# Optimization experiments

Hardware: AMD Instinct MI355X
Metric: run time of the kernel (lower is better)

## Reference

```python
import jax, jax.numpy as jnp
import numpy as np

T, A, C = 32, 64, 3            # steps, image side (A==B), channels
RN, WN = 5, 5                  # read/write glimpse sizes
Z, ENC, DEC = 100, 512, 512    # latent, encoder, decoder sizes
LIN, LH, AL = 300, 128, 512    # lang input, lang hidden, align hidden
BATCH, L = 128, 32             # batch, caption length


def lstm_cell(xt, h, c, Wih, Whh, bih, bhh):
    # torch.nn.LSTMCell gate order: i, f, g, o
    g = xt @ Wih.T + h @ Whh.T + bih + bhh
    i, f, gg, o = jnp.split(g, 4, axis=-1)
    c2 = jax.nn.sigmoid(f) * c + jax.nn.sigmoid(i) * jnp.tanh(gg)
    return jax.nn.sigmoid(o) * jnp.tanh(c2), c2


def bi_lstm(y, Wf, Uf, bf1, bf2, Wb, Ub, bb1, bb2):
    Bsz, H = y.shape[0], Uf.shape[1]
    xs = jnp.swapaxes(y, 0, 1)  # [L,B,LIN]
    z = jnp.zeros((Bsz, H), y.dtype)
    def mk(Wih, Whh, bih, bhh):
        def step(carry, xt):
            h, c = carry
            h2, c2 = lstm_cell(xt, h, c, Wih, Whh, bih, bhh)
            return (h2, c2), h2
        return step
    _, hf = jax.lax.scan(mk(Wf, Uf, bf1, bf2), (z, z), xs)
    _, hb = jax.lax.scan(mk(Wb, Ub, bb1, bb2), (z, z), xs, reverse=True)
    return jnp.concatenate([jnp.swapaxes(hf, 0, 1), jnp.swapaxes(hb, 0, 1)], axis=-1)


def filterbank(gx, gy, sigma2, delta, N):
    grid = jnp.arange(N, dtype=jnp.float32)[None]          # [1,N]
    mu_x = gx + (grid - N / 2 - 0.5) * delta               # [b,N]
    mu_y = gy + (grid - N / 2 - 0.5) * delta
    a = jnp.arange(A, dtype=jnp.float32)                   # [A] (A==B)
    s2 = sigma2[:, :, None]                                # [b,1,1]
    Fx = jnp.exp(-(a[None, None, :] - mu_x[:, :, None]) ** 2 / (2 * s2))
    Fy = jnp.exp(-(a[None, None, :] - mu_y[:, :, None]) ** 2 / (2 * s2))
    Fx = Fx / (Fx.sum(2, keepdims=True) + 1e-8)
    Fy = Fy / (Fy.sum(2, keepdims=True) + 1e-8)
    return Fx, Fy                                          # [b,N,A]


def attn_window(h, W, b, N):
    p = h @ W.T + b                                        # [b,5]
    gx_, gy_, ls2, ld, lg = [p[:, i:i + 1] for i in range(5)]
    gx = (A + 1) / 2 * (gx_ + 1)
    gy = (A + 1) / 2 * (gy_ + 1)
    delta = (A - 1) / (N - 1) * jnp.exp(ld)
    Fx, Fy = filterbank(gx, gy, jnp.exp(ls2), delta, N)
    return Fx, Fy, jnp.exp(lg)


def setup_inputs() -> dict:
    key = jax.random.key(0)
    ki = iter(jax.random.split(key, 64))
    def p(shape, s=0.05):
        return s * jax.random.normal(next(ki), shape, dtype=jnp.float32)
    z = lambda *s: jnp.zeros(s, jnp.float32)
    inp = {}
    inp['x'] = jax.random.uniform(next(ki), (BATCH, C * A * A), dtype=jnp.float32)
    inp['y'] = p((BATCH, L, LIN), 1.0)
    inp['eps_q'] = p((T, BATCH, Z), 1.0)
    inp['enc_Wih'] = p((4 * ENC, 2 * RN * RN * C + DEC)); inp['enc_Whh'] = p((4 * ENC, ENC))
    inp['enc_bih'] = z(4 * ENC); inp['enc_bhh'] = z(4 * ENC)
    inp['dec_Wih'] = p((4 * DEC, Z + 2 * LH)); inp['dec_Whh'] = p((4 * DEC, DEC))
    inp['dec_bih'] = z(4 * DEC); inp['dec_bhh'] = z(4 * DEC)
    inp['mu_W'] = p((Z, ENC)); inp['mu_b'] = z(Z)
    inp['sig_W'] = p((Z, ENC)); inp['sig_b'] = z(Z)
    inp['write_W'] = p((WN * WN * C, DEC)); inp['write_b'] = z(WN * WN * C)
    inp['align_W1'] = p((AL, 2 * LH + DEC)); inp['align_b1'] = z(AL)
    inp['align_w2'] = p((1, AL))
    inp['attn_W'] = p((5, DEC)); inp['attn_b'] = z(5)
    inp['lf_Wih'] = p((4 * LH, LIN)); inp['lf_Whh'] = p((4 * LH, LH))
    inp['lf_bih'] = z(4 * LH); inp['lf_bhh'] = z(4 * LH)
    inp['lb_Wih'] = p((4 * LH, LIN)); inp['lb_Whh'] = p((4 * LH, LH))
    inp['lb_bih'] = z(4 * LH); inp['lb_bhh'] = z(4 * LH)
    return inp


def reference(x, y, eps_q, enc_Wih, enc_Whh, enc_bih, enc_bhh, dec_Wih, dec_Whh,
              dec_bih, dec_bhh, mu_W, mu_b, sig_W, sig_b, write_W, write_b,
              align_W1, align_b1, align_w2, attn_W, attn_b,
              lf_Wih, lf_Whh, lf_bih, lf_bhh, lb_Wih, lb_Whh, lb_bih, lb_bhh):
    Bsz = x.shape[0]
    h_lang = bi_lstm(y, lf_Wih, lf_Whh, lf_bih, lf_bhh, lb_Wih, lb_Whh, lb_bih, lb_bhh)  # [b,L,2LH]
    x_img = x.reshape(Bsz, C, A, A)
    # original code never updates c_prev for t>0 (no-op line), so c_prev == 0 always
    xhat_img = x_img - 0.5  # x - sigmoid(0)

    def step(carry, eps):
        h_enc, c_enc, h_dec, c_dec = carry
        # read glimpse with Gaussian filterbank from previous decoder state
        Fx, Fy, gamma = attn_window(h_dec, attn_W, attn_b, RN)
        def glimpse(img):
            g = jnp.einsum('biy,bcyx,bjx->bcij', Fy, img, Fx)  # [b,C,RN,RN]
            return g.reshape(Bsz, RN * RN * C) * gamma
        r = jnp.concatenate([glimpse(x_img), glimpse(xhat_img)], axis=1)
        h_enc2, c_enc2 = lstm_cell(jnp.concatenate([r, h_dec], 1), h_enc, c_enc,
                                   enc_Wih, enc_Whh, enc_bih, enc_bhh)
        mu = h_enc2 @ mu_W.T + mu_b
        q = mu + eps * jnp.exp(h_enc2 @ sig_W.T + sig_b)
        # alignment attention over language states (exp/normalize == softmax)
        ain = jnp.concatenate([jnp.broadcast_to(h_dec[:, None, :], (Bsz, h_lang.shape[1], DEC)), h_lang], -1)
        logits = jnp.tanh(ain @ align_W1.T + align_b1) @ align_w2.T  # [b,L,1]
        sent = jnp.sum(h_lang * jax.nn.softmax(logits, axis=1), axis=1)
        h_dec2, c_dec2 = lstm_cell(jnp.concatenate([q, sent], 1), h_dec, c_dec,
                                   dec_Wih, dec_Whh, dec_bih, dec_bhh)
        # write glimpse
        w = (h_dec2 @ write_W.T + write_b).reshape(Bsz, C, WN, WN)
        Fxw, Fyw, gw = attn_window(h_dec2, attn_W, attn_b, WN)
        wr = jnp.einsum('biy,bcij,bjx->bcyx', Fyw, w, Fxw).reshape(Bsz, C * A * A) / gw
        return (h_enc2, c_enc2, h_dec2, c_dec2), wr  # cs[t] = 0 + write

    ze = jnp.zeros((Bsz, ENC), x.dtype)
    zd = jnp.zeros((Bsz, DEC), x.dtype)
    _, cs = jax.lax.scan(step, (ze, ze, zd, zd), eps_q)
    return cs  # [T, b, C*A*A]
```

## Files before the change

kernel.cpp:

```cpp
#include <hip/hip_runtime.h>
#include <hip/hip_bf16.h>
#include <math.h>

typedef __attribute__((ext_vector_type(8))) short short8;
typedef __attribute__((ext_vector_type(4))) float floatx4;

__device__ __forceinline__ float sigmoidf_(float v){ return 1.f/(1.f+expf(-v)); }

__device__ __forceinline__ floatx4 mfma16(short8 a, short8 b, floatx4 c) {
    return __builtin_amdgcn_mfma_f32_16x16x32_bf16(a, b, c, 0, 0, 0);
}

__device__ __forceinline__ void store3(__hip_bfloat16* p, long row, int kp, int col, float v){
    __hip_bfloat16 hi = __float2bfloat16(v);
    float lo = v - __bfloat162float(hi);
    p[row + col]        = hi;
    p[row + kp + col]   = __float2bfloat16(lo);
    p[row + 2*kp + col] = hi;
}

#define MFMA_TILE_BODY \
    { const short8* A8 = (const short8*)sA; \
      const short8* B8 = (const short8*)sB; \
      short8 a0 = A8[l], a1 = A8[64+l]; \
      short8 b0 = B8[(w*2)*64 + l], b1 = B8[(w*2+1)*64 + l]; \
      acc[0][0] = mfma16(a0,b0,acc[0][0]); \
      acc[0][1] = mfma16(a0,b1,acc[0][1]); \
      acc[1][0] = mfma16(a1,b0,acc[1][0]); \
      acc[1][1] = mfma16(a1,b1,acc[1][1]); }

#define MFMA_TILE_BODY2 \
    { const short8* A8 = (const short8*)sA; \
      const short8* B8 = (const short8*)sB; \
      short8 a0 = A8[l], a1 = A8[64+l]; \
      short8 b0 = B8[(w*2)*64 + l], b1 = B8[(w*2+1)*64 + l]; \
      acc[0][0] = mfma16(a0,b0,acc[0][0]); \
      acc[0][1] = mfma16(a0,b1,acc[0][1]); \
      acc[1][0] = mfma16(a1,b0,acc[1][0]); \
      acc[1][1] = mfma16(a1,b1,acc[1][1]); \
      short8 c0 = A8[128+l], c1 = A8[192+l]; \
      short8 d0 = B8[512+(w*2)*64 + l], d1 = B8[512+(w*2+1)*64 + l]; \
      acc[0][0] = mfma16(c0,d0,acc[0][0]); \
      acc[0][1] = mfma16(c0,d1,acc[0][1]); \
      acc[1][0] = mfma16(c1,d0,acc[1][0]); \
      acc[1][1] = mfma16(c1,d1,acc[1][1]); }

__device__ void mfma_loop_32x128(const __hip_bfloat16* Apk, long lda, int m0,
                                 const __hip_bfloat16* Wrows, long ldb,
                                 int KS, char* sA, char* sB, floatx4 acc[2][2])
{
    const int tid = threadIdx.x, l = tid & 63, w = tid >> 6;
    const char* Ab = (const char*)(Apk + (long)(m0 + (tid>>6)*16 + (tid&15))*lda
                                   + (long)(((tid&63)>>4)*8));
    int r0 = tid >> 2, qd = tid & 3;
    const char* Bb0 = (const char*)(Wrows + (long)r0*ldb + qd*8);
    const char* Bb1 = (const char*)(Wrows + (long)(r0+64)*ldb + qd*8);
    int4* sAv = (int4*)sA;
    int4* sBv = (int4*)sB;
    int bs0 = (r0>>4)*64 + (r0&15) + (qd<<4);
    int bs1 = bs0 + 256;
    const int NIT = KS >> 1, tail = KS & 1;
    int4 aE0,aE1,b0E0,b0E1,b1E0,b1E1;
    int4 aO0,aO1,b0O0,b0O1,b1O0,b1O1;
    if (NIT > 0) {
        if (tid < 128) { aE0 = *(const int4*)Ab; aE1 = *(const int4*)(Ab+64); }
        b0E0 = *(const int4*)Bb0; b0E1 = *(const int4*)(Bb0+64);
        b1E0 = *(const int4*)Bb1; b1E1 = *(const int4*)(Bb1+64);
    }
    if (NIT > 1) {
        if (tid < 128) { aO0 = *(const int4*)(Ab+128); aO1 = *(const int4*)(Ab+192); }
        b0O0 = *(const int4*)(Bb0+128); b0O1 = *(const int4*)(Bb0+192);
        b1O0 = *(const int4*)(Bb1+128); b1O1 = *(const int4*)(Bb1+192);
    }
    int it = 0;
    for (; it + 1 < NIT; it += 2) {
        __syncthreads();
        if (tid < 128) { sAv[tid] = aE0; sAv[128+tid] = aE1; }
        sBv[bs0] = b0E0; sBv[bs1] = b1E0; sBv[512+bs0] = b0E1; sBv[512+bs1] = b1E1;
        __syncthreads();
        if (it + 2 < NIT) {
            long off = (long)(it+2)*128;
            if (tid < 128) { aE0 = *(const int4*)(Ab+off); aE1 = *(const int4*)(Ab+off+64); }
            b0E0 = *(const int4*)(Bb0+off); b0E1 = *(const int4*)(Bb0+off+64);
            b1E0 = *(const int4*)(Bb1+off); b1E1 = *(const int4*)(Bb1+off+64);
        }
        MFMA_TILE_BODY2
        __syncthreads();
        if (tid < 128) { sAv[tid] = aO0; sAv[128+tid] = aO1; }
        sBv[bs0] = b0O0; sBv[bs1] = b1O0; sBv[512+bs0] = b0O1; sBv[512+bs1] = b1O1;
        __syncthreads();
        if (it + 3 < NIT) {
            long off = (long)(it+3)*128;
            if (tid < 128) { aO0 = *(const int4*)(Ab+off); aO1 = *(const int4*)(Ab+off+64); }
            b0O0 = *(const int4*)(Bb0+off); b0O1 = *(const int4*)(Bb0+off+64);
            b1O0 = *(const int4*)(Bb1+off); b1O1 = *(const int4*)(Bb1+off+64);
        }
        MFMA_TILE_BODY2
    }
    if (it < NIT) {
        __syncthreads();
        if (tid < 128) { sAv[tid] = aE0; sAv[128+tid] = aE1; }
        sBv[bs0] = b0E0; sBv[bs1] = b1E0; sBv[512+bs0] = b0E1; sBv[512+bs1] = b1E1;
        __syncthreads();
        MFMA_TILE_BODY2
    }
    if (tail) {
        long off = (long)NIT*128;
        int4 aT, bT0, bT1;
        if (tid < 128) aT = *(const int4*)(Ab+off);
        bT0 = *(const int4*)(Bb0+off); bT1 = *(const int4*)(Bb1+off);
        __syncthreads();
        if (tid < 128) sAv[tid] = aT;
        sBv[bs0] = bT0; sBv[bs1] = bT1;
        __syncthreads();
        MFMA_TILE_BODY
    }
}

__device__ void gemm_tile(const __hip_bfloat16* Apk, long lda, int m0,
                          const __hip_bfloat16* Wpk, long ldb, int n0,
                          const float* b1, const float* b2,
                          void* Cout, long ldc, int KS, int out_bf16, char* smem)
{
    char* sA = smem; char* sB = smem + 4096;
    floatx4 z4 = {0.f,0.f,0.f,0.f};
    floatx4 acc[2][2] = {{z4,z4},{z4,z4}};
    mfma_loop_32x128(Apk, lda, m0, Wpk + (long)n0*ldb, ldb, KS, sA, sB, acc);
    const int tid = threadIdx.x, l = tid&63, w = tid>>6;
    for (int i = 0; i < 2; ++i)
      for (int jn = 0; jn < 2; ++jn) {
        int n = n0 + (w*2+jn)*16 + (l&15);
        float bb = (b1? b1[n]:0.f) + (b2? b2[n]:0.f);
        for (int r = 0; r < 4; ++r) {
            int m = m0 + i*16 + ((l>>4)<<2) + r;
            float v = acc[i][jn][r] + bb;
            if (out_bf16) ((__hip_bfloat16*)Cout)[(long)m*ldc + n] = __float2bfloat16(v);
            else          ((float*)Cout)[(long)m*ldc + n] = v;
        }
      }
}

__global__ __launch_bounds__(256)
void gemm_mfma_k(const __hip_bfloat16* Apk, long lda,
                 const __hip_bfloat16* Bpk, long ldb,
                 const float* b1, const float* b2,
                 void* Cout, long ldc, int KS, int out_bf16)
{
    __shared__ __align__(16) char smem[20480];
    gemm_tile(Apk, lda, blockIdx.x*32, Bpk, ldb, blockIdx.y*128, b1, b2,
              Cout, ldc, KS, out_bf16, smem);
}

__device__ void gates_cell_tile(const __hip_bfloat16* Apk, long lda,
                                const __hip_bfloat16* Wpk, long ldw,
                                const float* bpk, float* c_state, float* h_f32,
                                __hip_bfloat16* d1, int d1ld, int d1kp, int d1off,
                                __hip_bfloat16* d2, int d2ld, int d2kp, int d2off,
                                __hip_bfloat16* d3, int d3ld, int d3kp, int d3off,
                                int KS, int m0, int jb, char* smem)
{
    char* sA = smem; char* sB = smem + 4096;
    floatx4 z4 = {0.f,0.f,0.f,0.f};
    floatx4 acc[2][2] = {{z4,z4},{z4,z4}};
    mfma_loop_32x128(Apk, lda, m0, Wpk + (long)jb*128*ldw, ldw, KS, sA, sB, acc);
    __syncthreads();
    float (*gl)[36] = (float(*)[36])smem;
    const int tid = threadIdx.x, l = tid&63, w = tid>>6;
    for (int i = 0; i < 2; ++i)
      for (int jn = 0; jn < 2; ++jn) {
        int nl = (w*2+jn)*16 + (l&15);
        int mb = i*16 + ((l>>4)<<2);
        *(floatx4*)&gl[nl][mb] = acc[i][jn];
      }
    __syncthreads();
    for (int idx = tid; idx < 1024; idx += 256) {
        int u = idx >> 5, m = idx & 31;
        float g0 = gl[u   ][m] + bpk[jb*128 + u];
        float g1 = gl[32+u][m] + bpk[jb*128 + 32 + u];
        float g2 = gl[64+u][m] + bpk[jb*128 + 64 + u];
        float g3 = gl[96+u][m] + bpk[jb*128 + 96 + u];
        int bg = m0 + m, un = jb*32 + u;
        long ci = (long)bg*512 + un;
        float c2 = sigmoidf_(g1)*c_state[ci] + sigmoidf_(g0)*tanhf(g2);
        float h2 = sigmoidf_(g3)*tanhf(c2);
        c_state[ci] = c2;
        if (h_f32) h_f32[ci] = h2;
        store3(d1, (long)bg*d1ld, d1kp, d1off + un, h2);
        if (d2) store3(d2, (long)bg*d2ld, d2kp, d2off + un, h2);
        if (d3) store3(d3, (long)bg*d3ld, d3kp, d3off + un, h2);
    }
}

__device__ void align_fn(int b, const float* dp, const float* langpre,
                         const float* hlang, const float* w2,
                         __hip_bfloat16* Ad_p, char* smem)
{
    float* dps    = (float*)smem;
    float* red    = dps + 512;
    float* logits = red + 256;
    float* smv    = logits + 32;
    float* ssum   = smv + 32;
    const int tid = threadIdx.x;
    for (int k = tid; k < 512; k += 256) dps[k] = dp[(long)b*512 + k];
    __syncthreads();
    {
        int ll = tid >> 3, part = tid & 7;
        const float* lp = langpre + ((long)b*32 + ll)*512 + part*64;
        const float* dpp = dps + part*64;
        const float* w2p = w2 + part*64;
        float acc = 0.f;
        for (int a = 0; a < 64; ++a)
            acc += tanhf(dpp[a] + lp[a]) * w2p[a];
        red[tid] = acc;
    }
    __syncthreads();
    if ((tid & 7) == 0) {
        float s = 0.f;
        for (int p2 = 0; p2 < 8; ++p2) s += red[tid + p2];
        logits[tid >> 3] = s;
    }
    __syncthreads();
    if (tid == 0) {
        float mx = logits[0];
        for (int i = 1; i < 32; ++i) mx = fmaxf(mx, logits[i]);
        float s = 0.f;
        for (int i = 0; i < 32; ++i) { float e = expf(logits[i]-mx); smv[i]=e; s+=e; }
        ssum[0] = s;
    }
    __syncthreads();
    {
        float acc = 0.f;
        const float* hl = hlang + (long)b*32*256 + tid;
        for (int i = 0; i < 32; ++i) acc += smv[i]*hl[(long)i*256];
        store3(Ad_p, (long)b*2688, 896, 104 + tid, acc/ssum[0]);
    }
}

__global__ __launch_bounds__(256)
void enc_align_k(const __hip_bfloat16* Ae_p, const __hip_bfloat16* Wenc,
                 const float* benc, float* c_enc,
                 __hip_bfloat16* Ae_q, __hip_bfloat16* Ahe3,
                 const float* dp, const float* langpre, const float* hlang,
                 const float* w2, __hip_bfloat16* Ad_p)
{
    __shared__ __align__(16) char smem[20480];
    int bid = blockIdx.x;
    if (bid < 64) {
        int m0 = ((bid>>4)&3)*32, jb = bid & 15;
        gates_cell_tile(Ae_p, 3552, Wenc, 3552, benc, c_enc, nullptr,
                        Ae_q, 3552, 1184, 664,  Ahe3, 1536, 512, 0,
                        nullptr, 0, 0, 0,  111, m0, jb, smem);
    } else {
        align_fn(bid-64, dp, langpre, hlang, w2, Ad_p, smem);
    }
}

__global__ __launch_bounds__(256)
void dec_k(const __hip_bfloat16* Ad_p, const __hip_bfloat16* Wdec, const float* bdec,
           float* c_dec, float* h_dec,
           __hip_bfloat16* Ae_q, __hip_bfloat16* Ad_q, __hip_bfloat16* Ahd3)
{
    __shared__ __align__(16) char smem[20480];
    int m0 = ((blockIdx.x>>4)&3)*32, jb = blockIdx.x & 15;
    gates_cell_tile(Ad_p, 2688, Wdec, 2688, bdec, c_dec, h_dec,
                    Ae_q, 3552, 1184, 152,  Ad_q, 2688, 896, 360,
                    Ahd3, 1536, 512, 0,  84, m0, jb, smem);
}

__global__ __launch_bounds__(256)
void musig_k(const __hip_bfloat16* Ahe3, const __hip_bfloat16* Wms3,
             const float* mu_b, const float* sig_b,
             const float* eps, __hip_bfloat16* Ad_p)
{
    __shared__ __align__(16) char smem[20480];
    char* sA = smem; char* sB = smem + 4096;
    floatx4 z4 = {0.f,0.f,0.f,0.f};
    floatx4 acc[2][2] = {{z4,z4},{z4,z4}};
    int m0 = blockIdx.x*32, n0 = blockIdx.y*128, base = blockIdx.y*64;
    mfma_loop_32x128(Ahe3, 1536, m0, Wms3 + (long)n0*1536, 1536, 48, sA, sB, acc);
    __syncthreads();
    float (*gl)[36] = (float(*)[36])smem;
    const int tid = threadIdx.x, l = tid&63, w = tid>>6;
    for (int i = 0; i < 2; ++i)
      for (int jn = 0; jn < 2; ++jn) {
        int nl = (w*2+jn)*16 + (l&15);
        int mb = i*16 + ((l>>4)<<2);
        *(floatx4*)&gl[nl][mb] = acc[i][jn];
      }
    __syncthreads();
    for (int idx = tid; idx < 2048; idx += 256) {
        int u = idx >> 5, m = idx & 31;
        int o = base + u;
        if (o >= 100) continue;
        int bg = m0 + m;
        float mu = gl[u][m] + mu_b[o];
        float sg = expf(gl[64+u][m] + sig_b[o]);
        float q = mu + eps[(long)bg*100 + o]*sg;
        store3(Ad_p, (long)bg*2688, 896, o, q);
    }
}

__device__ void attn_params5(const float* hd, const float* attn_W, const float* attn_b,
                             float* sP, float* scratch)
{
    const int tid = threadIdx.x;
    float p0=0.f,p1=0.f,p2=0.f,p3=0.f,p4=0.f;
    for (int k = tid; k < 512; k += 256) {
        float v = hd[k];
        p0 += v*attn_W[k];      p1 += v*attn_W[512+k];  p2 += v*attn_W[1024+k];
        p3 += v*attn_W[1536+k]; p4 += v*attn_W[2048+k];
    }
    for (int off = 32; off; off >>= 1) {
        p0 += __shfl_down(p0, off); p1 += __shfl_down(p1, off);
        p2 += __shfl_down(p2, off); p3 += __shfl_down(p3, off);
        p4 += __shfl_down(p4, off);
    }
    if ((tid & 63) == 0) {
        int wv = tid >> 6;
        scratch[wv*5+0]=p0; scratch[wv*5+1]=p1; scratch[wv*5+2]=p2;
        scratch[wv*5+3]=p3; scratch[wv*5+4]=p4;
    }
    __syncthreads();
    if (tid < 5) sP[tid] = scratch[tid]+scratch[5+tid]+scratch[10+tid]+scratch[15+tid]+attn_b[tid];
    __syncthreads();
}

__device__ void glimpse_fn(int b, const float* x, const float* h_dec,
                           const float* attn_W, const float* attn_b,
                           __hip_bfloat16* Ae_q, char* smem)
{
    float* red = (float*)smem;
    float* sP  = red + 256;
    float* Fx  = sP + 8;
    float* Fy  = Fx + 320;
    float* denx= Fy + 320;
    float* deny= denx + 8;
    float* SFx = deny + 8;
    float* SFy = SFx + 8;
    float* tmp1= SFy + 8;
    const int tid = threadIdx.x;
    attn_params5(h_dec + (long)b*512, attn_W, attn_b, sP, red);
    float gx    = 32.5f*(sP[0]+1.f);
    float gy    = 32.5f*(sP[1]+1.f);
    float s2    = expf(sP[2]);
    float delta = 15.75f*expf(sP[3]);
    for (int p = tid; p < 320; p += 256) {
        int i = p >> 6, a = p & 63;
        float mux = gx + ((float)i - 3.0f)*delta;
        float muy = gy + ((float)i - 3.0f)*delta;
        float dx = (float)a - mux, dy = (float)a - muy;
        Fx[i*64+a] = expf(-dx*dx/(2.f*s2));
        Fy[i*64+a] = expf(-dy*dy/(2.f*s2));
    }
    __syncthreads();
    if (tid < 10) {
        int i = tid % 5;
        const float* F = (tid < 5) ? (Fx + i*64) : (Fy + i*64);
        float s = 0.f;
        for (int a = 0; a < 64; ++a) s += F[a];
        if (tid < 5) denx[i] = s + 1e-8f; else deny[i] = s + 1e-8f;
    }
    __syncthreads();
    for (int p = tid; p < 320; p += 256) {
        int i = p >> 6, a = p & 63;
        Fx[i*64+a] /= denx[i];
        Fy[i*64+a] /= deny[i];
    }
    __syncthreads();
    if (tid < 10) {
        int i = tid % 5;
        const float* F = (tid < 5) ? (Fx + i*64) : (Fy + i*64);
        float s = 0.f;
        for (int a = 0; a < 64; ++a) s += F[a];
        if (tid < 5) SFx[i] = s; else SFy[i] = s;
    }
    __syncthreads();
    for (int p = tid; p < 192; p += 256) {
        int cc = p / 64, yy = p - cc*64;
        const float* row = x + (long)b*12288 + cc*4096 + yy*64;
        float a0=0,a1=0,a2=0,a3=0,a4=0;
        for (int xx = 0; xx < 64; ++xx) {
            float v = row[xx];
            a0 += v*Fx[0*64+xx]; a1 += v*Fx[1*64+xx]; a2 += v*Fx[2*64+xx];
            a3 += v*Fx[3*64+xx]; a4 += v*Fx[4*64+xx];
        }
        tmp1[(cc*64+yy)*5+0]=a0; tmp1[(cc*64+yy)*5+1]=a1; tmp1[(cc*64+yy)*5+2]=a2;
        tmp1[(cc*64+yy)*5+3]=a3; tmp1[(cc*64+yy)*5+4]=a4;
    }
    __syncthreads();
    if (tid < 75) {
        int cc = tid/25, i = (tid/5)%5, j = tid%5;
        float g = 0.f;
        for (int yy = 0; yy < 64; ++yy) g += Fy[i*64+yy]*tmp1[(cc*64+yy)*5 + j];
        float gamma = expf(sP[4]);
        long ro = (long)b*3552;
        store3(Ae_q, ro, 1184, tid,      gamma*g);
        store3(Ae_q, ro, 1184, 75 + tid, gamma*(g - 0.5f*SFy[i]*SFx[j]));
    }
}

__device__ void write_fn(int b, const float* h_dec,
                         const float* write_W, const float* write_b,
                         const float* attn_W, const float* attn_b,
                         float* outp, char* smem)
{
    float* hs  = (float*)smem;
    float* red = hs + 512;
    float* sP  = red + 256;
    float* w75 = sP + 8;
    float* Fx  = w75 + 80;
    float* Fy  = Fx + 320;
    float* denx= Fy + 320;
    float* deny= denx + 8;
    float* t2  = deny + 8;
    const int tid = threadIdx.x;
    for (int k = tid; k < 512; k += 256) hs[k] = h_dec[(long)b*512 + k];
    __syncthreads();
    attn_params5(hs, attn_W, attn_b, sP, red);
    float gx    = 32.5f*(sP[0]+1.f);
    float gy    = 32.5f*(sP[1]+1.f);
    float s2    = expf(sP[2]);
    float delta = 15.75f*expf(sP[3]);
    float inv_g = 1.f/expf(sP[4]);
    if (tid < 75) {
        const float4* w4 = (const float4*)(write_W + (long)tid*512);
        const float4* h4 = (const float4*)hs;
        float acc = 0.f;
        for (int k = 0; k < 128; ++k) {
            float4 wv = w4[k], hv = h4[k];
            acc += wv.x*hv.x + wv.y*hv.y + wv.z*hv.z + wv.w*hv.w;
        }
        w75[tid] = acc + write_b[tid];
    }
    for (int p = tid; p < 320; p += 256) {
        int i = p >> 6, a = p & 63;
        float mux = gx + ((float)i - 3.0f)*delta;
        float muy = gy + ((float)i - 3.0f)*delta;
        float dx = (float)a - mux, dy = (float)a - muy;
        Fx[i*64+a] = expf(-dx*dx/(2.f*s2));
        Fy[i*64+a] = expf(-dy*dy/(2.f*s2));
    }
    __syncthreads();
    if (tid < 10) {
        int i = tid % 5;
        const float* F = (tid < 5) ? (Fx + i*64) : (Fy + i*64);
        float s = 0.f;
        for (int a = 0; a < 64; ++a) s += F[a];
        if (tid < 5) denx[i] = s + 1e-8f; else deny[i] = s + 1e-8f;
    }
    __syncthreads();
    for (int p = tid; p < 320; p += 256) {
        int i = p >> 6, a = p & 63;
        Fx[i*64+a] /= denx[i];
        Fy[i*64+a] /= deny[i];
    }
    __syncthreads();
    for (int p = tid; p < 960; p += 256) {
        int cc = p / 320, rem = p - cc*320;
        int i = rem / 64, xx = rem - i*64;
        float acc = 0.f;
        for (int j = 0; j < 5; ++j) acc += w75[cc*25 + i*5 + j]*Fx[j*64+xx];
        t2[(cc*5+i)*64+xx] = acc;
    }
    __syncthreads();
    float* ob = outp + (long)b*12288;
    for (int p = tid; p < 12288; p += 256) {
        int cc = p >> 12, yy = (p >> 6) & 63, xx = p & 63;
        float acc = 0.f;
        for (int i = 0; i < 5; ++i) acc += Fy[i*64+yy]*t2[(cc*5+i)*64+xx];
        ob[p] = acc*inv_g;
    }
}

__global__ __launch_bounds__(256)
void wgd_k(const float* x, const float* h_dec,
           const float* attn_W, const float* attn_b,
           const float* write_W, const float* write_b,
           float* outp,
           __hip_bfloat16* Ae_q,
           const __hip_bfloat16* Ahd3, const __hip_bfloat16* W1dec3,
           float* dp)
{
    __shared__ __align__(16) char smem[20480];
    int bid = blockIdx.x;
    if (bid < 128) {
        glimpse_fn(bid, x, h_dec, attn_W, attn_b, Ae_q, smem);
    } else if (bid < 144) {
        int t = bid - 128;
        gemm_tile(Ahd3, 1536, (t&3)*32, W1dec3, 1536, (t>>2)*128,
                  nullptr, nullptr, dp, 512, 48, 0, smem);
    } else {
        if (outp) write_fn(bid-144, h_dec, write_W, write_b, attn_W, attn_b, outp, smem);
    }
}

__global__ __launch_bounds__(512)
void lang_all_k(const float* xpf, const float* xpb,
                const float* Whh_f, const float* Whh_b,
                float* hlang)
{
    const int pr  = blockIdx.x & 63;
    const int dir = blockIdx.x >> 6;
    const int tid = threadIdx.x;
    const int b0  = pr*2;
    const float* Whh = dir ? Whh_b : Whh_f;
    const float* xps = dir ? xpb : xpf;
    __shared__ __align__(16) float hs[2][128];
    __shared__ float gs[2][512];
    float4 wr[32];
    {
        const float4* w4 = (const float4*)(Whh + (long)tid*128);
        #pragma unroll
        for (int k = 0; k < 32; ++k) wr[k] = w4[k];
    }
    if (tid < 256) hs[tid>>7][tid&127] = 0.f;
    float cst = 0.f;
    __syncthreads();
    for (int s = 0; s < 32; ++s) {
        const int l = dir ? (31 - s) : s;
        const float4* h40 = (const float4*)hs[0];
        const float4* h41 = (const float4*)hs[1];
        float a0 = 0.f, a1 = 0.f;
        #pragma unroll
        for (int k = 0; k < 32; ++k) {
            float4 wv = wr[k], h0 = h40[k], h1 = h41[k];
            a0 += wv.x*h0.x + wv.y*h0.y + wv.z*h0.z + wv.w*h0.w;
            a1 += wv.x*h1.x + wv.y*h1.y + wv.z*h1.z + wv.w*h1.w;
        }
        gs[0][tid] = a0 + xps[((long)b0*32 + l)*512 + tid];
        gs[1][tid] = a1 + xps[((long)(b0+1)*32 + l)*512 + tid];
        __syncthreads();
        if (tid < 256) {
            int bb = tid >> 7, u = tid & 127;
            float c2 = sigmoidf_(gs[bb][128+u])*cst + sigmoidf_(gs[bb][u])*tanhf(gs[bb][256+u]);
            float h2 = sigmoidf_(gs[bb][384+u])*tanhf(c2);
            cst = c2;
            hlang[((long)(b0+bb)*32 + l)*256 + dir*128 + u] = h2;
            hs[bb][u] = h2;
        }
        __syncthreads();
    }
}

__global__ void pack_a3_k(__hip_bfloat16* dst, int KP, long N,
                          const float* src, int ld, int K1)
{
    long idx = (long)blockIdx.x*256 + threadIdx.x;
    int K3 = 3*KP;
    long tot = N*K3;
    if (idx >= tot) return;
    long n = idx / K3; int k3 = (int)(idx - n*K3);
    int plane = k3 / KP, k = k3 - plane*KP;
    float v = (k < K1) ? src[n*ld + k] : 0.f;
    __hip_bfloat16 hi = __float2bfloat16(v);
    float lo = v - __bfloat162float(hi);
    dst[idx] = (plane==1) ? __float2bfloat16(lo) : hi;
}

__global__ void pack_w3_k(__hip_bfloat16* dst, int KP, long N,
                          const float* src, int ld, int K1)
{
    long idx = (long)blockIdx.x*256 + threadIdx.x;
    int K3 = 3*KP;
    long tot = N*K3;
    if (idx >= tot) return;
    long n = idx / K3; int k3 = (int)(idx - n*K3);
    int plane = k3 / KP, k = k3 - plane*KP;
    float v = (k < K1) ? src[n*ld + k] : 0.f;
    __hip_bfloat16 hi = __float2bfloat16(v);
    float lo = v - __bfloat162float(hi);
    dst[idx] = (plane==2) ? __float2bfloat16(lo) : hi;
}

__global__ void pack_gates3_k(__hip_bfloat16* dst, int KP,
                              const float* Wih, int ldih, int K1, int off2, int K2, int off3,
                              const float* Whh)
{
    long idx = (long)blockIdx.x*256 + threadIdx.x;
    int K3 = 3*KP;
    long tot = 2048L*K3;
    if (idx >= tot) return;
    long p = idx / K3; int k3 = (int)(idx - p*K3);
    int plane = k3 / KP, k = k3 - plane*KP;
    int j = (int)(p >> 7), g = (int)((p>>5)&3), uu = (int)(p&31);
    int n = g*512 + j*32 + uu;
    float v = 0.f;
    if (k < K1)                          v = Wih[(long)n*ldih + k];
    else if (k >= off2 && k < off2+K2)   v = Wih[(long)n*ldih + K1 + (k-off2)];
    else if (k >= off3 && k < off3+512)  v = Whh[(long)n*512 + (k-off3)];
    __hip_bfloat16 hi = __float2bfloat16(v);
    float lo = v - __bfloat162float(hi);
    dst[idx] = (plane==2) ? __float2bfloat16(lo) : hi;
}

__global__ void pack_gbias_k(float* dst, const float* bih, const float* bhh)
{
    int p = blockIdx.x*256 + threadIdx.x;
    if (p >= 2048) return;
    int j = p >> 7, g = (p>>5)&3, uu = p&31;
    int n = g*512 + j*32 + uu;
    dst[p] = bih[n] + bhh[n];
}

__global__ void pack_musig3_k(__hip_bfloat16* dst, const float* mu_W, const float* sig_W)
{
    long idx = (long)blockIdx.x*256 + threadIdx.x;
    if (idx >= 256L*1536) return;
    int p = (int)(idx / 1536), k3 = (int)(idx - (long)p*1536);
    int plane = k3 >> 9, k = k3 & 511;
    int u = p & 127, base = (p >> 7)*64;
    int z = base + (u & 63);
    const float* W = (u < 64) ? mu_W : sig_W;
    float v = (z < 100) ? W[(long)z*512 + k] : 0.f;
    __hip_bfloat16 hi = __float2bfloat16(v);
    float lo = v - __bfloat162float(hi);
    dst[idx] = (plane==2) ? __float2bfloat16(lo) : hi;
}

extern "C" void kernel_launch(void* const* d_in, const int* in_sizes, int n_in,
                              void* d_out, int out_size, void* d_ws, size_t ws_size,
                              hipStream_t stream)
{
    const float* x        = (const float*)d_in[0];
    const float* y        = (const float*)d_in[1];
    const float* eps_q    = (const float*)d_in[2];
    const float* enc_Wih  = (const float*)d_in[3];
    const float* enc_Whh  = (const float*)d_in[4];
    const float* enc_bih  = (const float*)d_in[5];
    const float* enc_bhh  = (const float*)d_in[6];
    const float* dec_Wih  = (const float*)d_in[7];
    const float* dec_Whh  = (const float*)d_in[8];
    const float* dec_bih  = (const float*)d_in[9];
    const float* dec_bhh  = (const float*)d_in[10];
    const float* mu_W     = (const float*)d_in[11];
    const float* mu_b     = (const float*)d_in[12];
    const float* sig_W    = (const float*)d_in[13];
    const float* sig_b    = (const float*)d_in[14];
    const float* write_W  = (const float*)d_in[15];
    const float* write_b  = (const float*)d_in[16];
    const float* align_W1 = (const float*)d_in[17];
    const float* align_b1 = (const float*)d_in[18];
    const float* align_w2 = (const float*)d_in[19];
    const float* attn_W   = (const float*)d_in[20];
    const float* attn_b   = (const float*)d_in[21];
    const float* lf_Wih   = (const float*)d_in[22];
    const float* lf_Whh   = (const float*)d_in[23];
    const float* lf_bih   = (const float*)d_in[24];
    const float* lf_bhh   = (const float*)d_in[25];
    const float* lb_Wih   = (const float*)d_in[26];
    const float* lb_Whh   = (const float*)d_in[27];
    const float* lb_bih   = (const float*)d_in[28];
    const float* lb_bhh   = (const float*)d_in[29];
    float* out = (float*)d_out;

    float* ws = (float*)d_ws;
    size_t off = 0;
    auto alloc = [&](size_t n){ float* p = ws + off; off += n; return p; };

    float* Aenc0f = alloc(227328);
    float* Aenc1f = alloc(227328);
    float* Adec0f = alloc(172032);
    float* Adec1f = alloc(172032);
    float* Ahd3f  = alloc(98304);
    float* Ahe3f  = alloc(98304);
    float* c_enc  = alloc(65536);
    float* c_dec  = alloc(65536);
    float* h_dec  = alloc(65536);
    size_t zero_floats = off;
    float* dpb      = alloc(65536);
    float* hlangf   = alloc(1048576);
    float* hlang3f  = alloc(1572864);
    float* langpre  = alloc(2097152);
    float* W1lang3f = alloc(196608);
    float* W1dec3f  = alloc(393216);
    float* shared = alloc(6651904);
    float* y3f   = shared;
    float* Wlf3f = shared + 1966080;
    float* Wlb3f = Wlf3f + 245760;
    float* xpf   = Wlb3f + 245760;
    float* xpb   = xpf + 2097152;
    float* Wenc3f = shared;
    float* Wdec3f = Wenc3f + 3637248;
    float* Wms3f  = Wdec3f + 2752512;
    float* benc   = Wms3f + 196608;
    float* bdec   = benc + 2048;

    __hip_bfloat16* Aenc0 = (__hip_bfloat16*)Aenc0f;
    __hip_bfloat16* Aenc1 = (__hip_bfloat16*)Aenc1f;
    __hip_bfloat16* Adec0 = (__hip_bfloat16*)Adec0f;
    __hip_bfloat16* Adec1 = (__hip_bfloat16*)Adec1f;
    __hip_bfloat16* Ahd3  = (__hip_bfloat16*)Ahd3f;
    __hip_bfloat16* Ahe3  = (__hip_bfloat16*)Ahe3f;
    __hip_bfloat16* hlang3= (__hip_bfloat16*)hlang3f;
    __hip_bfloat16* W1lang3=(__hip_bfloat16*)W1lang3f;
    __hip_bfloat16* W1dec3= (__hip_bfloat16*)W1dec3f;
    __hip_bfloat16* y3    = (__hip_bfloat16*)y3f;
    __hip_bfloat16* Wlf3  = (__hip_bfloat16*)Wlf3f;
    __hip_bfloat16* Wlb3  = (__hip_bfloat16*)Wlb3f;
    __hip_bfloat16* Wenc3 = (__hip_bfloat16*)Wenc3f;
    __hip_bfloat16* Wdec3 = (__hip_bfloat16*)Wdec3f;
    __hip_bfloat16* Wms3  = (__hip_bfloat16*)Wms3f;

    hipMemsetAsync(ws, 0, zero_floats*sizeof(float), stream);

    pack_a3_k<<<(4096L*960+255)/256,256,0,stream>>>(y3, 320, 4096, y, 300, 300);
    pack_w3_k<<<(512L*960+255)/256,256,0,stream>>>(Wlf3, 320, 512, lf_Wih, 300, 300);
    pack_w3_k<<<(512L*960+255)/256,256,0,stream>>>(Wlb3, 320, 512, lb_Wih, 300, 300);
    pack_w3_k<<<(512L*768+255)/256,256,0,stream>>>(W1lang3, 256, 512, align_W1+512, 768, 256);
    pack_w3_k<<<(512L*1536+255)/256,256,0,stream>>>(W1dec3, 512, 512, align_W1, 768, 512);
    gemm_mfma_k<<<dim3(128,4),256,0,stream>>>(y3, 960, Wlf3, 960, lf_bih, lf_bhh, xpf, 512, 30, 0);
    gemm_mfma_k<<<dim3(128,4),256,0,stream>>>(y3, 960, Wlb3, 960, lb_bih, lb_bhh, xpb, 512, 30, 0);
    lang_all_k<<<128,512,0,stream>>>(xpf, xpb, lf_Whh, lb_Whh, hlangf);
    pack_a3_k<<<(4096L*768+255)/256,256,0,stream>>>(hlang3, 256, 4096, hlangf, 256, 256);
    gemm_mfma_k<<<dim3(128,4),256,0,stream>>>(hlang3, 768, W1lang3, 768, align_b1, nullptr, langpre, 512, 24, 0);

    pack_gates3_k<<<(2048L*10656+255)/256,256,0,stream>>>(Wenc3, 1184, enc_Wih, 662, 150, 152, 512, 664, enc_Whh);
    pack_gates3_k<<<(2048L*8064+255)/256,256,0,stream>>>(Wdec3, 896, dec_Wih, 356, 100, 104, 256, 360, dec_Whh);
    pack_gbias_k<<<8,256,0,stream>>>(benc, enc_bih, enc_bhh);
    pack_gbias_k<<<8,256,0,stream>>>(bdec, dec_bih, dec_bhh);
    pack_musig3_k<<<(256L*1536+255)/256,256,0,stream>>>(Wms3, mu_W, sig_W);

    wgd_k<<<272,256,0,stream>>>(x, h_dec, attn_W, attn_b, write_W, write_b,
                                nullptr, Aenc0, Ahd3, W1dec3, dpb);

    for (int t = 0; t < 32; ++t) {
        int p = t & 1;
        __hip_bfloat16* Ae_p = p ? Aenc1 : Aenc0;
        __hip_bfloat16* Ae_q = p ? Aenc0 : Aenc1;
        __hip_bfloat16* Ad_p = p ? Adec1 : Adec0;
        __hip_bfloat16* Ad_q = p ? Adec0 : Adec1;
        enc_align_k<<<192,256,0,stream>>>(Ae_p, Wenc3, benc, c_enc, Ae_q, Ahe3,
                                          dpb, langpre, hlangf, align_w2, Ad_p);
        musig_k<<<dim3(4,2),256,0,stream>>>(Ahe3, Wms3, mu_b, sig_b,
                                            eps_q + (long)t*12800, Ad_p);
        dec_k<<<64,256,0,stream>>>(Ad_p, Wdec3, bdec, c_dec, h_dec, Ae_q, Ad_q, Ahd3);
        wgd_k<<<272,256,0,stream>>>(x, h_dec, attn_W, attn_b, write_W, write_b,
                                    out + (long)t*128*12288, Ae_q, Ahd3, W1dec3, dpb);
    }
}
```

Measured before the change: 4.117 ms.

## Split-K the recurrent LSTM gate and mu/sigma GEMMs across two blocks

The encoder, decoder and mu/sigma GEMM tiles now split K across two blocks. Each block writes its partial accumulators to global memory, and an atomic counter picks the last-arriving block to add the other half and run the epilogue. This doubles the number of blocks per step in the latency-bound recurrent loop, at the cost of partial-sum traffic, fences and per-step counter arrays. The glimpse read loop is also vectorized with float4 loads, and the pack kernels use a 2D grid so the per-element 64-bit divisions go away.

```diff
diff --git a/kernel.cpp b/kernel.cpp
--- a/kernel.cpp
+++ b/kernel.cpp
@@ -117,6 +117,30 @@
     }
 }
 
+__device__ int splitk_handoff(floatx4 acc[2][2], float* partial, int* cnt,
+                              int tile, int half)
+{
+    const int tid = threadIdx.x;
+    float* pb = partial + ((long)tile*2 + half)*4096 + tid*16;
+    *(floatx4*)(pb)    = acc[0][0];
+    *(floatx4*)(pb+4)  = acc[0][1];
+    *(floatx4*)(pb+8)  = acc[1][0];
+    *(floatx4*)(pb+12) = acc[1][1];
+    __threadfence();
+    __shared__ int who;
+    __syncthreads();
+    if (tid == 0) who = atomicAdd(&cnt[tile], 1);
+    __syncthreads();
+    if (who == 0) return 0;
+    __threadfence();
+    const float* ob = partial + ((long)tile*2 + (1-half))*4096 + tid*16;
+    acc[0][0] += *(const floatx4*)(ob);
+    acc[0][1] += *(const floatx4*)(ob+4);
+    acc[1][0] += *(const floatx4*)(ob+8);
+    acc[1][1] += *(const floatx4*)(ob+12);
+    return 1;
+}
+
 __device__ void gemm_tile(const __hip_bfloat16* Apk, long lda, int m0,
                           const __hip_bfloat16* Wpk, long ldb, int n0,
                           const float* b1, const float* b2,
@@ -157,12 +181,19 @@
                                 __hip_bfloat16* d1, int d1ld, int d1kp, int d1off,
                                 __hip_bfloat16* d2, int d2ld, int d2kp, int d2off,
                                 __hip_bfloat16* d3, int d3ld, int d3kp, int d3off,
-                                int KS, int m0, int jb, char* smem)
+                                int KS_all, int KS0, int half,
+                                float* partial, int* cnt,
+                                int m0, int jb, char* smem)
 {
     char* sA = smem; char* sB = smem + 4096;
     floatx4 z4 = {0.f,0.f,0.f,0.f};
     floatx4 acc[2][2] = {{z4,z4},{z4,z4}};
-    mfma_loop_32x128(Apk, lda, m0, Wpk + (long)jb*128*ldw, ldw, KS, sA, sB, acc);
+    long kofs = half ? (long)KS0*32 : 0;
+    int KS = half ? (KS_all - KS0) : KS0;
+    mfma_loop_32x128(Apk + kofs, lda, m0, Wpk + (long)jb*128*ldw + kofs, ldw,
+                     KS, sA, sB, acc);
+    int tile = ((m0>>5)<<4) + jb;
+    if (!splitk_handoff(acc, partial, cnt, tile, half)) return;
     __syncthreads();
     float (*gl)[36] = (float(*)[36])smem;
     const int tid = threadIdx.x, l = tid&63, w = tid>>6;
@@ -241,43 +272,55 @@
                  const float* benc, float* c_enc,
                  __hip_bfloat16* Ae_q, __hip_bfloat16* Ahe3,
                  const float* dp, const float* langpre, const float* hlang,
-                 const float* w2, __hip_bfloat16* Ad_p)
+                 const float* w2, __hip_bfloat16* Ad_p,
+                 float* partial, int* cnt)
 {
     __shared__ __align__(16) char smem[20480];
     int bid = blockIdx.x;
-    if (bid < 64) {
-        int m0 = ((bid>>4)&3)*32, jb = bid & 15;
+    if (bid < 128) {
+        int half = bid & 1, tl = bid >> 1;
+        int m0 = ((tl>>4)&3)*32, jb = tl & 15;
         gates_cell_tile(Ae_p, 3552, Wenc, 3552, benc, c_enc, nullptr,
                         Ae_q, 3552, 1184, 664,  Ahe3, 1536, 512, 0,
-                        nullptr, 0, 0, 0,  111, m0, jb, smem);
+                        nullptr, 0, 0, 0,
+                        111, 56, half, partial, cnt, m0, jb, smem);
     } else {
-        align_fn(bid-64, dp, langpre, hlang, w2, Ad_p, smem);
+        align_fn(bid-128, dp, langpre, hlang, w2, Ad_p, smem);
     }
 }
 
 __global__ __launch_bounds__(256)
 void dec_k(const __hip_bfloat16* Ad_p, const __hip_bfloat16* Wdec, const float* bdec,
            float* c_dec, float* h_dec,
-           __hip_bfloat16* Ae_q, __hip_bfloat16* Ad_q, __hip_bfloat16* Ahd3)
+           __hip_bfloat16* Ae_q, __hip_bfloat16* Ad_q, __hip_bfloat16* Ahd3,
+           float* partial, int* cnt)
 {
     __shared__ __align__(16) char smem[20480];
-    int m0 = ((blockIdx.x>>4)&3)*32, jb = blockIdx.x & 15;
+    int half = blockIdx.x & 1, tl = blockIdx.x >> 1;
+    int m0 = ((tl>>4)&3)*32, jb = tl & 15;
     gates_cell_tile(Ad_p, 2688, Wdec, 2688, bdec, c_dec, h_dec,
                     Ae_q, 3552, 1184, 152,  Ad_q, 2688, 896, 360,
-                    Ahd3, 1536, 512, 0,  84, m0, jb, smem);
+                    Ahd3, 1536, 512, 0,
+                    84, 42, half, partial, cnt, m0, jb, smem);
 }
 
 __global__ __launch_bounds__(256)
 void musig_k(const __hip_bfloat16* Ahe3, const __hip_bfloat16* Wms3,
              const float* mu_b, const float* sig_b,
-             const float* eps, __hip_bfloat16* Ad_p)
+             const float* eps, __hip_bfloat16* Ad_p,
+             float* partial, int* cnt)
 {
     __shared__ __align__(16) char smem[20480];
     char* sA = smem; char* sB = smem + 4096;
     floatx4 z4 = {0.f,0.f,0.f,0.f};
     floatx4 acc[2][2] = {{z4,z4},{z4,z4}};
     int m0 = blockIdx.x*32, n0 = blockIdx.y*128, base = blockIdx.y*64;
-    mfma_loop_32x128(Ahe3, 1536, m0, Wms3 + (long)n0*1536, 1536, 48, sA, sB, acc);
+    int half = blockIdx.z;
+    long kofs = half ? 24L*32 : 0;
+    mfma_loop_32x128(Ahe3 + kofs, 1536, m0, Wms3 + (long)n0*1536 + kofs, 1536,
+                     24, sA, sB, acc);
+    int tile = blockIdx.x*2 + blockIdx.y;
+    if (!splitk_handoff(acc, partial, cnt, tile, half)) return;
     __syncthreads();
     float (*gl)[36] = (float(*)[36])smem;
     const int tid = threadIdx.x, l = tid&63, w = tid>>6;
@@ -377,12 +420,17 @@
     __syncthreads();
     for (int p = tid; p < 192; p += 256) {
         int cc = p / 64, yy = p - cc*64;
-        const float* row = x + (long)b*12288 + cc*4096 + yy*64;
+        const float4* row4 = (const float4*)(x + (long)b*12288 + cc*4096 + yy*64);
         float a0=0,a1=0,a2=0,a3=0,a4=0;
-        for (int xx = 0; xx < 64; ++xx) {
-            float v = row[xx];
-            a0 += v*Fx[0*64+xx]; a1 += v*Fx[1*64+xx]; a2 += v*Fx[2*64+xx];
-            a3 += v*Fx[3*64+xx]; a4 += v*Fx[4*64+xx];
+        #pragma unroll
+        for (int q4 = 0; q4 < 16; ++q4) {
+            float4 v = row4[q4];
+            int xx = q4*4;
+            a0 += v.x*Fx[xx]     + v.y*Fx[xx+1]     + v.z*Fx[xx+2]     + v.w*Fx[xx+3];
+            a1 += v.x*Fx[64+xx]  + v.y*Fx[64+xx+1]  + v.z*Fx[64+xx+2]  + v.w*Fx[64+xx+3];
+            a2 += v.x*Fx[128+xx] + v.y*Fx[128+xx+1] + v.z*Fx[128+xx+2] + v.w*Fx[128+xx+3];
+            a3 += v.x*Fx[192+xx] + v.y*Fx[192+xx+1] + v.z*Fx[192+xx+2] + v.w*Fx[192+xx+3];
+            a4 += v.x*Fx[256+xx] + v.y*Fx[256+xx+1] + v.z*Fx[256+xx+2] + v.w*Fx[256+xx+3];
         }
         tmp1[(cc*64+yy)*5+0]=a0; tmp1[(cc*64+yy)*5+1]=a1; tmp1[(cc*64+yy)*5+2]=a2;
         tmp1[(cc*64+yy)*5+3]=a3; tmp1[(cc*64+yy)*5+4]=a4;
@@ -542,47 +590,47 @@
     }
 }
 
-__global__ void pack_a3_k(__hip_bfloat16* dst, int KP, long N,
+__global__ void pack_a3_k(__hip_bfloat16* dst, int KP,
                           const float* src, int ld, int K1)
 {
-    long idx = (long)blockIdx.x*256 + threadIdx.x;
+    int k3 = blockIdx.x*256 + threadIdx.x;
     int K3 = 3*KP;
-    long tot = N*K3;
-    if (idx >= tot) return;
-    long n = idx / K3; int k3 = (int)(idx - n*K3);
-    int plane = k3 / KP, k = k3 - plane*KP;
+    if (k3 >= K3) return;
+    long n = blockIdx.y;
+    int plane = (k3 >= KP) + (k3 >= 2*KP);
+    int k = k3 - plane*KP;
     float v = (k < K1) ? src[n*ld + k] : 0.f;
     __hip_bfloat16 hi = __float2bfloat16(v);
     float lo = v - __bfloat162float(hi);
-    dst[idx] = (plane==1) ? __float2bfloat16(lo) : hi;
-}
-
-__global__ void pack_w3_k(__hip_bfloat16* dst, int KP, long N,
+    dst[n*K3 + k3] = (plane==1) ? __float2bfloat16(lo) : hi;
+}
+
+__global__ void pack_w3_k(__hip_bfloat16* dst, int KP,
                           const float* src, int ld, int K1)
 {
-    long idx = (long)blockIdx.x*256 + threadIdx.x;
+    int k3 = blockIdx.x*256 + threadIdx.x;
     int K3 = 3*KP;
-    long tot = N*K3;
-    if (idx >= tot) return;
-    long n = idx / K3; int k3 = (int)(idx - n*K3);
-    int plane = k3 / KP, k = k3 - plane*KP;
+    if (k3 >= K3) return;
+    long n = blockIdx.y;
+    int plane = (k3 >= KP) + (k3 >= 2*KP);
+    int k = k3 - plane*KP;
     float v = (k < K1) ? src[n*ld + k] : 0.f;
     __hip_bfloat16 hi = __float2bfloat16(v);
     float lo = v - __bfloat162float(hi);
-    dst[idx] = (plane==2) ? __float2bfloat16(lo) : hi;
+    dst[n*K3 + k3] = (plane==2) ? __float2bfloat16(lo) : hi;
 }
 
 __global__ void pack_gates3_k(__hip_bfloat16* dst, int KP,
                               const float* Wih, int ldih, int K1, int off2, int K2, int off3,
                               const float* Whh)
 {
-    long idx = (long)blockIdx.x*256 + threadIdx.x;
+    int k3 = blockIdx.x*256 + threadIdx.x;
     int K3 = 3*KP;
-    long tot = 2048L*K3;
-    if (idx >= tot) return;
-    long p = idx / K3; int k3 = (int)(idx - p*K3);
-    int plane = k3 / KP, k = k3 - plane*KP;
-    int j = (int)(p >> 7), g = (int)((p>>5)&3), uu = (int)(p&31);
+    if (k3 >= K3) return;
+    int p = blockIdx.y;
+    int plane = (k3 >= KP) + (k3 >= 2*KP);
+    int k = k3 - plane*KP;
+    int j = p >> 7, g = (p>>5)&3, uu = p&31;
     int n = g*512 + j*32 + uu;
     float v = 0.f;
     if (k < K1)                          v = Wih[(long)n*ldih + k];
@@ -590,7 +638,7 @@
     else if (k >= off3 && k < off3+512)  v = Whh[(long)n*512 + (k-off3)];
     __hip_bfloat16 hi = __float2bfloat16(v);
     float lo = v - __bfloat162float(hi);
-    dst[idx] = (plane==2) ? __float2bfloat16(lo) : hi;
+    dst[(long)p*K3 + k3] = (plane==2) ? __float2bfloat16(lo) : hi;
 }
 
 __global__ void pack_gbias_k(float* dst, const float* bih, const float* bhh)
@@ -604,9 +652,9 @@
 
 __global__ void pack_musig3_k(__hip_bfloat16* dst, const float* mu_W, const float* sig_W)
 {
-    long idx = (long)blockIdx.x*256 + threadIdx.x;
-    if (idx >= 256L*1536) return;
-    int p = (int)(idx / 1536), k3 = (int)(idx - (long)p*1536);
+    int k3 = blockIdx.x*256 + threadIdx.x;
+    if (k3 >= 1536) return;
+    int p = blockIdx.y;
     int plane = k3 >> 9, k = k3 & 511;
     int u = p & 127, base = (p >> 7)*64;
     int z = base + (u & 63);
@@ -614,7 +662,7 @@
     float v = (z < 100) ? W[(long)z*512 + k] : 0.f;
     __hip_bfloat16 hi = __float2bfloat16(v);
     float lo = v - __bfloat162float(hi);
-    dst[idx] = (plane==2) ? __float2bfloat16(lo) : hi;
+    dst[(long)p*1536 + k3] = (plane==2) ? __float2bfloat16(lo) : hi;
 }
 
 extern "C" void kernel_launch(void* const* d_in, const int* in_sizes, int n_in,
@@ -666,6 +714,9 @@
     float* c_enc  = alloc(65536);
     float* c_dec  = alloc(65536);
     float* h_dec  = alloc(65536);
+    int*   enc_cnt = (int*)alloc(2048);
+    int*   dec_cnt = (int*)alloc(2048);
+    int*   ms_cnt  = (int*)alloc(256);
     size_t zero_floats = off;
     float* dpb      = alloc(65536);
     float* hlangf   = alloc(1048576);
@@ -673,6 +724,9 @@
     float* langpre  = alloc(2097152);
     float* W1lang3f = alloc(196608);
     float* W1dec3f  = alloc(393216);
+    float* enc_part = alloc(524288);
+    float* dec_part = alloc(524288);
+    float* ms_part  = alloc(65536);
     float* shared = alloc(6651904);
     float* y3f   = shared;
     float* Wlf3f = shared + 1966080;
@@ -703,22 +757,22 @@
 
     hipMemsetAsync(ws, 0, zero_floats*sizeof(float), stream);
 
-    pack_a3_k<<<(4096L*960+255)/256,256,0,stream>>>(y3, 320, 4096, y, 300, 300);
-    pack_w3_k<<<(512L*960+255)/256,256,0,stream>>>(Wlf3, 320, 512, lf_Wih, 300, 300);
-    pack_w3_k<<<(512L*960+255)/256,256,0,stream>>>(Wlb3, 320, 512, lb_Wih, 300, 300);
-    pack_w3_k<<<(512L*768+255)/256,256,0,stream>>>(W1lang3, 256, 512, align_W1+512, 768, 256);
-    pack_w3_k<<<(512L*1536+255)/256,256,0,stream>>>(W1dec3, 512, 512, align_W1, 768, 512);
+    pack_a3_k<<<dim3(4,4096),256,0,stream>>>(y3, 320, y, 300, 300);
+    pack_w3_k<<<dim3(4,512),256,0,stream>>>(Wlf3, 320, lf_Wih, 300, 300);
+    pack_w3_k<<<dim3(4,512),256,0,stream>>>(Wlb3, 320, lb_Wih, 300, 300);
+    pack_w3_k<<<dim3(3,512),256,0,stream>>>(W1lang3, 256, align_W1+512, 768, 256);
+    pack_w3_k<<<dim3(6,512),256,0,stream>>>(W1dec3, 512, align_W1, 768, 512);
     gemm_mfma_k<<<dim3(128,4),256,0,stream>>>(y3, 960, Wlf3, 960, lf_bih, lf_bhh, xpf, 512, 30, 0);
     gemm_mfma_k<<<dim3(128,4),256,0,stream>>>(y3, 960, Wlb3, 960, lb_bih, lb_bhh, xpb, 512, 30, 0);
     lang_all_k<<<128,512,0,stream>>>(xpf, xpb, lf_Whh, lb_Whh, hlangf);
-    pack_a3_k<<<(4096L*768+255)/256,256,0,stream>>>(hlang3, 256, 4096, hlangf, 256, 256);
+    pack_a3_k<<<dim3(3,4096),256,0,stream>>>(hlang3, 256, hlangf, 256, 256);
     gemm_mfma_k<<<dim3(128,4),256,0,stream>>>(hlang3, 768, W1lang3, 768, align_b1, nullptr, langpre, 512, 24, 0);
 
-    pack_gates3_k<<<(2048L*10656+255)/256,256,0,stream>>>(Wenc3, 1184, enc_Wih, 662, 150, 152, 512, 664, enc_Whh);
-    pack_gates3_k<<<(2048L*8064+255)/256,256,0,stream>>>(Wdec3, 896, dec_Wih, 356, 100, 104, 256, 360, dec_Whh);
+    pack_gates3_k<<<dim3(42,2048),256,0,stream>>>(Wenc3, 1184, enc_Wih, 662, 150, 152, 512, 664, enc_Whh);
+    pack_gates3_k<<<dim3(32,2048),256,0,stream>>>(Wdec3, 896, dec_Wih, 356, 100, 104, 256, 360, dec_Whh);
     pack_gbias_k<<<8,256,0,stream>>>(benc, enc_bih, enc_bhh);
     pack_gbias_k<<<8,256,0,stream>>>(bdec, dec_bih, dec_bhh);
-    pack_musig3_k<<<(256L*1536+255)/256,256,0,stream>>>(Wms3, mu_W, sig_W);
+    pack_musig3_k<<<dim3(6,256),256,0,stream>>>(Wms3, mu_W, sig_W);
 
     wgd_k<<<272,256,0,stream>>>(x, h_dec, attn_W, attn_b, write_W, write_b,
                                 nullptr, Aenc0, Ahd3, W1dec3, dpb);
@@ -729,11 +783,14 @@
         __hip_bfloat16* Ae_q = p ? Aenc0 : Aenc1;
         __hip_bfloat16* Ad_p = p ? Adec1 : Adec0;
         __hip_bfloat16* Ad_q = p ? Adec0 : Adec1;
-        enc_align_k<<<192,256,0,stream>>>(Ae_p, Wenc3, benc, c_enc, Ae_q, Ahe3,
-                                          dpb, langpre, hlangf, align_w2, Ad_p);
-        musig_k<<<dim3(4,2),256,0,stream>>>(Ahe3, Wms3, mu_b, sig_b,
-                                            eps_q + (long)t*12800, Ad_p);
-        dec_k<<<64,256,0,stream>>>(Ad_p, Wdec3, bdec, c_dec, h_dec, Ae_q, Ad_q, Ahd3);
+        enc_align_k<<<256,256,0,stream>>>(Ae_p, Wenc3, benc, c_enc, Ae_q, Ahe3,
+                                          dpb, langpre, hlangf, align_w2, Ad_p,
+                                          enc_part, enc_cnt + t*64);
+        musig_k<<<dim3(4,2,2),256,0,stream>>>(Ahe3, Wms3, mu_b, sig_b,
+                                              eps_q + (long)t*12800, Ad_p,
+                                              ms_part, ms_cnt + t*8);
+        dec_k<<<128,256,0,stream>>>(Ad_p, Wdec3, bdec, c_dec, h_dec, Ae_q, Ad_q, Ahd3,
+                                    dec_part, dec_cnt + t*64);
         wgd_k<<<272,256,0,stream>>>(x, h_dec, attn_W, attn_b, write_W, write_b,
                                     out + (long)t*128*12288, Ae_q, Ahd3, W1dec3, dpb);
     }
```

Result: slower. 4.673 ms (+13.5%).
